# Kernel optimization log

Measured on AMD Instinct MI355X. Metric: run time of the kernel, lower is better.

Reference implementation:

```python
import jax, jax.numpy as jnp
import numpy as np

HEAD_SIZE = 128
N_EMBD = 64
B, T = 8, 4096


def setup_inputs() -> dict:
    key = jax.random.key(0)
    k1, k2, k3, k4 = jax.random.split(key, 4)
    x = jax.random.normal(k1, (B, T, N_EMBD), dtype=jnp.float32)
    Wq = jax.random.normal(k2, (N_EMBD, HEAD_SIZE), dtype=jnp.float32) * (N_EMBD ** -0.5)
    Wk = jax.random.normal(k3, (N_EMBD, HEAD_SIZE), dtype=jnp.float32) * (N_EMBD ** -0.5)
    Wv = jax.random.normal(k4, (N_EMBD, HEAD_SIZE), dtype=jnp.float32) * (N_EMBD ** -0.5)
    return {"x": x, "Wq": Wq, "Wk": Wk, "Wv": Wv}


def reference(x, Wq, Wk, Wv):
    # x: [B, T, C]; single-head causal self-attention (nanoGPT Head)
    q = x @ Wq  # [B, T, H]
    k = x @ Wk  # [B, T, H]
    v = x @ Wv  # [B, T, H]
    scale = HEAD_SIZE ** -0.5
    scores = jnp.einsum("bth,bsh->bts", q, k) * scale  # [B, T, T]
    t = x.shape[1]
    causal = jnp.tril(jnp.ones((t, t), dtype=bool))  # [T, T]
    scores = jnp.where(causal[None, :, :], scores, jnp.float32(-jnp.inf))
    wei = jax.nn.softmax(scores, axis=-1)  # [B, T, T]; dropout p=0.0 -> identity
    out = jnp.einsum("bts,bsh->bth", wei, v)  # [B, T, H]
    return out
```

## Files before the change

kernel.cpp:

```cpp
#include <hip/hip_runtime.h>
#include <math.h>

#define BB 8
#define TT 4096
#define CC 64
#define HH 128
#define NTH 256
#define XSTR 72
#define WSTR 72
#define QSCALE ((float)(0.08838834764831845 * 1.4426950408889634))

typedef __attribute__((ext_vector_type(8)))  short short8;
typedef __attribute__((ext_vector_type(4)))  float floatx4;
typedef __attribute__((ext_vector_type(16))) float floatx16;

__device__ __forceinline__ unsigned short f2bf(float f) {
    union { float f; unsigned int u; } un; un.f = f;
    unsigned int r = un.u + 0x7FFF + ((un.u >> 16) & 1);
    return (unsigned short)(r >> 16);
}
__device__ __forceinline__ unsigned int pack2bf(float a, float b) {
    return (unsigned int)f2bf(a) | ((unsigned int)f2bf(b) << 16);
}
__device__ __forceinline__ float bflo(unsigned int u) {
    union { unsigned int u; float f; } x; x.u = u << 16; return x.f;
}
__device__ __forceinline__ float bfhi(unsigned int u) {
    union { unsigned int u; float f; } x; x.u = u & 0xffff0000u; return x.f;
}

__global__ __launch_bounds__(NTH) void qkv_mfma(
    const float* __restrict__ x,
    const float* __restrict__ Wq, const float* __restrict__ Wk, const float* __restrict__ Wv,
    unsigned short* __restrict__ qb, unsigned short* __restrict__ Kf,
    unsigned short* __restrict__ Vf)
{
    __shared__ __align__(16) unsigned short xs[64 * XSTR];
    __shared__ __align__(16) unsigned short Wts[3 * HH * WSTR];

    const int tid  = threadIdx.x;
    const int w    = tid >> 6;
    const int lane = tid & 63;
    const int quad = lane >> 4;
    const int lr   = lane & 15;

    const int b    = blockIdx.x >> 6;
    const int kblk = blockIdx.x & 63;
    const int t0   = kblk * 64;
    const long long rbase = (long long)b * TT + t0;

#pragma unroll
    for (int i = 0; i < 4; ++i) {
        const int idx = tid + i * NTH;
        const int r = idx >> 4, c4 = idx & 15;
        const float4 v = *(const float4*)(x + (rbase + r) * CC + c4 * 4);
        unsigned short tmp[4] = { f2bf(v.x), f2bf(v.y), f2bf(v.z), f2bf(v.w) };
        *(unsigned long long*)&xs[r * XSTR + c4 * 4] = *(unsigned long long*)tmp;
    }
#pragma unroll
    for (int mat = 0; mat < 3; ++mat) {
        const float* W = mat == 0 ? Wq : (mat == 1 ? Wk : Wv);
        const float s = mat == 0 ? QSCALE : 1.0f;
#pragma unroll
        for (int i = 0; i < 32; ++i) {
            const int idx = tid + i * NTH;
            const int c = idx >> 7, h = idx & 127;
            Wts[(mat * HH + h) * WSTR + c] = f2bf(W[idx] * s);
        }
    }
    __syncthreads();

    const short8 bx0 = *(const short8*)&xs[(w * 16 + lr) * XSTR + quad * 8];
    const short8 bx1 = *(const short8*)&xs[(w * 16 + lr) * XSTR + 32 + quad * 8];

    {
        const unsigned short* Wrow = Wts;
#pragma unroll
        for (int ht = 0; ht < 8; ++ht) {
            const short8 aw0 = *(const short8*)(Wrow + (ht * 16 + lr) * WSTR + quad * 8);
            const short8 aw1 = *(const short8*)(Wrow + (ht * 16 + lr) * WSTR + 32 + quad * 8);
            floatx4 acc = (floatx4)0.f;
            acc = __builtin_amdgcn_mfma_f32_16x16x32_bf16(aw0, bx0, acc, 0, 0, 0);
            acc = __builtin_amdgcn_mfma_f32_16x16x32_bf16(aw1, bx1, acc, 0, 0, 0);
            ushort4 st = { f2bf(acc[0]), f2bf(acc[1]), f2bf(acc[2]), f2bf(acc[3]) };
            *(ushort4*)(qb + (rbase + w * 16 + lr) * HH + ht * 16 + quad * 4) = st;
        }
    }
    {
        const unsigned short* Wrow = Wts + 1 * HH * WSTR;
        const int khp = w >> 1;
        const int lqp = (w & 1) * 16 + lr;
        unsigned short* kdst = Kf + ((long long)((b * 64 + kblk) * 2 + khp)) * 4096
                             + ((quad >> 1) & 1) * 256 + lqp * 8 + (quad & 1) * 4;
#pragma unroll
        for (int ht = 0; ht < 8; ++ht) {
            const short8 aw0 = *(const short8*)(Wrow + (ht * 16 + lr) * WSTR + quad * 8);
            const short8 aw1 = *(const short8*)(Wrow + (ht * 16 + lr) * WSTR + 32 + quad * 8);
            floatx4 acc = (floatx4)0.f;
            acc = __builtin_amdgcn_mfma_f32_16x16x32_bf16(aw0, bx0, acc, 0, 0, 0);
            acc = __builtin_amdgcn_mfma_f32_16x16x32_bf16(aw1, bx1, acc, 0, 0, 0);
            ushort4 st = { f2bf(acc[0]), f2bf(acc[1]), f2bf(acc[2]), f2bf(acc[3]) };
            *(ushort4*)(kdst + ht * 512) = st;
        }
    }
    {
        const unsigned short* Wrow = Wts + 2 * HH * WSTR;
        const int khv = w >> 1, ksv = w & 1, lsv = (quad >> 1) & 1;
        unsigned short* vdst = Vf + (long long)(b * 64 + kblk) * 8192 + khv * 4096
                             + ksv * 512 + lsv * 256 + (quad & 1) * 4;
#pragma unroll
        for (int htp = 0; htp < 8; ++htp) {
            const short8 bw0 = *(const short8*)(Wrow + (htp * 16 + lr) * WSTR + quad * 8);
            const short8 bw1 = *(const short8*)(Wrow + (htp * 16 + lr) * WSTR + 32 + quad * 8);
            floatx4 acc = (floatx4)0.f;
            acc = __builtin_amdgcn_mfma_f32_16x16x32_bf16(bx0, bw0, acc, 0, 0, 0);
            acc = __builtin_amdgcn_mfma_f32_16x16x32_bf16(bx1, bw1, acc, 0, 0, 0);
            ushort4 st = { f2bf(acc[0]), f2bf(acc[1]), f2bf(acc[2]), f2bf(acc[3]) };
            *(ushort4*)(vdst + (htp >> 1) * 1024 + ((htp & 1) * 16 + lr) * 8) = st;
        }
    }
}

__global__ __launch_bounds__(NTH, 2) void flash_splitk(
    const unsigned short* __restrict__ qb,
    const unsigned short* __restrict__ Kf,
    const unsigned short* __restrict__ Vf,
    unsigned short* __restrict__ Ob, float* __restrict__ Lb)
{
    __shared__ __align__(16) float ex[2][64 * 68];
    __shared__ float Lx[4][32];

    const int tid  = threadIdx.x;
    const int w    = tid >> 6;
    const int lane = tid & 63;
    const int lq   = lane & 31;
    const int ls   = lane >> 5;
    const int kh   = w & 1;
    const int qh   = w >> 1;

    const int id  = blockIdx.x;
    const int qt  = 63 - (id >> 5);
    const int b   = (id >> 2) & 7;
    const int c   = id & 3;
    const int len = (qt + 4) >> 2;
    const int lo  = c * len;
    if (lo > qt) return;
    const int hi  = (lo + len - 1 < qt) ? (lo + len - 1) : qt;

    const int q0 = qt * 64;
    const long long baset = (long long)b * TT;

    const unsigned short* kptr = Kf + ((long long)(b * 128 + kh)) * 4096 + lane * 8;
    const unsigned short* vptr = Vf + ((long long)b * 64) * 8192 + kh * 4096 + lane * 8;

    short8 aq[8];
    {
        const unsigned short* qrp = qb + (baset + q0 + qh * 32 + lq) * HH + ls * 8;
#pragma unroll
        for (int st = 0; st < 8; ++st)
            aq[st] = *(const short8*)(qrp + st * 16);
    }

    floatx16 o_acc[4];
#pragma unroll
    for (int ht = 0; ht < 4; ++ht) o_acc[ht] = (floatx16)0.f;
    float l_lane = 0.f;

    for (int kt = lo; kt <= hi; ++kt) {
        const unsigned short* kp = kptr + (long long)kt * 8192;
        const unsigned short* vp = vptr + (long long)kt * 8192;

        short8 kfr[8], vfr[8];
#pragma unroll
        for (int st = 0; st < 8; ++st)
            kfr[st] = *(const short8*)(kp + st * 512);
#pragma unroll
        for (int i = 0; i < 8; ++i)
            vfr[i] = *(const short8*)(vp + (i >> 1) * 1024 + (i & 1) * 512);

        const bool diag = (kt == qt);
        if (diag && kh > qh) continue;

        floatx16 s_acc = (floatx16)0.f;
#pragma unroll
        for (int st = 0; st < 8; ++st)
            s_acc = __builtin_amdgcn_mfma_f32_32x32x16_bf16(kfr[st], aq[st], s_acc, 0, 0, 0);

        float p[16];
        if (diag && kh == qh) {
#pragma unroll
            for (int reg = 0; reg < 16; ++reg) {
                const int kk = (reg & 3) + 8 * (reg >> 2) + 4 * ls;
                p[reg] = (kk <= lq) ? exp2f(s_acc[reg]) : 0.f;
            }
        } else {
#pragma unroll
            for (int reg = 0; reg < 16; ++reg)
                p[reg] = exp2f(s_acc[reg]);
        }
#pragma unroll
        for (int reg = 0; reg < 16; ++reg) l_lane += p[reg];

        unsigned int g[8], pg[8];
#pragma unroll
        for (int i = 0; i < 8; ++i) g[i] = pack2bf(p[2 * i], p[2 * i + 1]);
#pragma unroll
        for (int i = 0; i < 8; ++i) pg[i] = __shfl_xor((int)g[i], 32);
        short8 bp[2];
#pragma unroll
        for (int ks = 0; ks < 2; ++ks) {
            union { short8 s; unsigned int u[4]; } fr;
            const int bs = ks * 4;
            if (ls == 0) {
                fr.u[0] = g[bs];      fr.u[1] = g[bs + 1];
                fr.u[2] = pg[bs];     fr.u[3] = pg[bs + 1];
            } else {
                fr.u[0] = pg[bs + 2]; fr.u[1] = pg[bs + 3];
                fr.u[2] = g[bs + 2];  fr.u[3] = g[bs + 3];
            }
            bp[ks] = fr.s;
        }

#pragma unroll
        for (int ht = 0; ht < 4; ++ht) {
            o_acc[ht] = __builtin_amdgcn_mfma_f32_32x32x16_bf16(vfr[ht * 2 + 0], bp[0], o_acc[ht], 0, 0, 0);
            o_acc[ht] = __builtin_amdgcn_mfma_f32_32x32x16_bf16(vfr[ht * 2 + 1], bp[1], o_acc[ht], 0, 0, 0);
        }
    }

    const float l2 = l_lane + __shfl_xor(l_lane, 32);
    if (lane < 32) Lx[w][lq] = l2;
    if (kh == 1) {
        float* e = &ex[qh][lane * 68];
#pragma unroll
        for (int ht = 0; ht < 4; ++ht)
#pragma unroll
            for (int rg = 0; rg < 4; ++rg) {
                float4 v = make_float4(o_acc[ht][rg * 4 + 0], o_acc[ht][rg * 4 + 1],
                                       o_acc[ht][rg * 4 + 2], o_acc[ht][rg * 4 + 3]);
                *(float4*)&e[ht * 16 + rg * 4] = v;
            }
    }
    __syncthreads();
    if (kh == 0) {
        const int pid = ((b * 64 + qt) << 2) + c;
        Lb[pid * 64 + qh * 32 + lq] = Lx[2 * qh][lq] + Lx[2 * qh + 1][lq];
        const float* e = &ex[qh][lane * 68];
        unsigned short* od = Ob + (long long)pid * 8192 + (qh * 32 + lq) * HH;
#pragma unroll
        for (int ht = 0; ht < 4; ++ht)
#pragma unroll
            for (int rg = 0; rg < 4; ++rg) {
                const float4 pv = *(const float4*)&e[ht * 16 + rg * 4];
                ushort4 st = { f2bf(o_acc[ht][rg * 4 + 0] + pv.x),
                               f2bf(o_acc[ht][rg * 4 + 1] + pv.y),
                               f2bf(o_acc[ht][rg * 4 + 2] + pv.z),
                               f2bf(o_acc[ht][rg * 4 + 3] + pv.w) };
                *(ushort4*)(od + ht * 32 + rg * 8 + 4 * ls) = st;
            }
    }
}

__global__ __launch_bounds__(NTH) void combine(
    const unsigned short* __restrict__ Ob, const float* __restrict__ Lb,
    float* __restrict__ out)
{
    const int id = blockIdx.x;
    const int b = id & 7, qt = id >> 3;
    const int len = (qt + 4) >> 2;
    const int tid = threadIdx.x;
    const int q = tid >> 2;
    const int hg = tid & 3;
    const int pid0 = (b * 64 + qt) << 2;

    float acc[32];
#pragma unroll
    for (int i = 0; i < 32; ++i) acc[i] = 0.f;
    float ltot = 0.f;

#pragma unroll
    for (int c = 0; c < 4; ++c) {
        if (c * len > qt) break;
        ltot += Lb[(pid0 + c) * 64 + q];
        const uint4* src = (const uint4*)(Ob + (long long)(pid0 + c) * 8192 + q * HH + hg * 32);
#pragma unroll
        for (int g = 0; g < 4; ++g) {
            const uint4 d = src[g];
            acc[g * 8 + 0] += bflo(d.x); acc[g * 8 + 1] += bfhi(d.x);
            acc[g * 8 + 2] += bflo(d.y); acc[g * 8 + 3] += bfhi(d.y);
            acc[g * 8 + 4] += bflo(d.z); acc[g * 8 + 5] += bfhi(d.z);
            acc[g * 8 + 6] += bflo(d.w); acc[g * 8 + 7] += bfhi(d.w);
        }
    }
    const float inv = 1.f / ltot;
    float* op = out + ((long long)b * TT + qt * 64 + q) * HH + hg * 32;
#pragma unroll
    for (int g = 0; g < 8; ++g) {
        float4 st = make_float4(acc[g * 4 + 0] * inv, acc[g * 4 + 1] * inv,
                                acc[g * 4 + 2] * inv, acc[g * 4 + 3] * inv);
        *(float4*)(op + g * 4) = st;
    }
}

extern "C" void kernel_launch(void* const* d_in, const int* in_sizes, int n_in,
                              void* d_out, int out_size, void* d_ws, size_t ws_size,
                              hipStream_t stream)
{
    const float* x  = (const float*)d_in[0];
    const float* Wq = (const float*)d_in[1];
    const float* Wk = (const float*)d_in[2];
    const float* Wv = (const float*)d_in[3];
    float* out = (float*)d_out;

    const long long n = (long long)BB * TT * HH;
    unsigned short* qb = (unsigned short*)d_ws;
    unsigned short* Kf = qb + n;
    unsigned short* Vf = Kf + n;
    unsigned short* Ob = Vf + n;
    float*          Lb = (float*)(Ob + (long long)2048 * 8192);

    qkv_mfma<<<BB * (TT / 64), NTH, 0, stream>>>(x, Wq, Wk, Wv, qb, Kf, Vf);
    flash_splitk<<<2048, NTH, 0, stream>>>(qb, Kf, Vf, Ob, Lb);
    combine<<<BB * 64, NTH, 0, stream>>>(Ob, Lb, out);
}
```

Baseline: 162.8 us.

## Double-buffer K/V tiles in LDS via async global-to-LDS loads with 128-row query tiles

The split-K flash kernel now uses 512-thread blocks covering 128 query rows, so each K/V tile is staged once into LDS and shared by twice as many query rows. Tiles are loaded with async global_load_lds into a double buffer, prefetching the next tile while the current one is computed. The causal mask is generalized to per-warp diagonal offsets, and the bf16 packing uses a cheaper perm-based round. The cost is more LDS per block, a barrier every iteration, and slightly different rounding on P and partial outputs.

```diff
diff --git a/kernel.cpp b/kernel.cpp
--- a/kernel.cpp
+++ b/kernel.cpp
@@ -19,14 +19,21 @@
     unsigned int r = un.u + 0x7FFF + ((un.u >> 16) & 1);
     return (unsigned short)(r >> 16);
 }
-__device__ __forceinline__ unsigned int pack2bf(float a, float b) {
-    return (unsigned int)f2bf(a) | ((unsigned int)f2bf(b) << 16);
+__device__ __forceinline__ unsigned int pack2bf_fast(float a, float b) {
+    union { float f; unsigned int u; } ua, ub; ua.f = a; ub.f = b;
+    return __builtin_amdgcn_perm(ub.u + 0x8000u, ua.u + 0x8000u, 0x07060302u);
 }
 __device__ __forceinline__ float bflo(unsigned int u) {
     union { unsigned int u; float f; } x; x.u = u << 16; return x.f;
 }
 __device__ __forceinline__ float bfhi(unsigned int u) {
     union { unsigned int u; float f; } x; x.u = u & 0xffff0000u; return x.f;
+}
+
+__device__ __forceinline__ void gl_lds16(const void* g, void* l) {
+    __builtin_amdgcn_global_load_lds(
+        (const __attribute__((address_space(1))) unsigned int*)g,
+        (__attribute__((address_space(3))) unsigned int*)l, 16, 0, 0);
 }
 
 __global__ __launch_bounds__(NTH) void qkv_mfma(
@@ -121,14 +128,32 @@
     }
 }
 
-__global__ __launch_bounds__(NTH, 2) void flash_splitk(
+__device__ __forceinline__ void dma_tile(
+    const unsigned char* __restrict__ Ksrc, const unsigned char* __restrict__ Vsrc,
+    long long kt, unsigned char* buf, int w, int lane)
+{
+    const unsigned char* src;
+    unsigned char* dst;
+    if (w < 4) {
+        src = Ksrc + kt * 16384 + w * 4096 + lane * 16;
+        dst = buf + w * 4096;
+    } else {
+        src = Vsrc + kt * 16384 + (w - 4) * 4096 + lane * 16;
+        dst = buf + 16384 + (w - 4) * 4096;
+    }
+#pragma unroll
+    for (int i = 0; i < 4; ++i)
+        gl_lds16(src + i * 1024, dst + i * 1024);
+}
+
+__global__ __launch_bounds__(512, 4) void flash_splitk(
     const unsigned short* __restrict__ qb,
     const unsigned short* __restrict__ Kf,
     const unsigned short* __restrict__ Vf,
     unsigned short* __restrict__ Ob, float* __restrict__ Lb)
 {
-    __shared__ __align__(16) float ex[2][64 * 68];
-    __shared__ float Lx[4][32];
+    __shared__ __align__(16) unsigned char KV[2][32768];
+    __shared__ float Lx[8][32];
 
     const int tid  = threadIdx.x;
     const int w    = tid >> 6;
@@ -138,20 +163,24 @@
     const int kh   = w & 1;
     const int qh   = w >> 1;
 
-    const int id  = blockIdx.x;
-    const int qt  = 63 - (id >> 5);
-    const int b   = (id >> 2) & 7;
-    const int c   = id & 3;
-    const int len = (qt + 4) >> 2;
-    const int lo  = c * len;
-    if (lo > qt) return;
-    const int hi  = (lo + len - 1 < qt) ? (lo + len - 1) : qt;
-
-    const int q0 = qt * 64;
+    const int id     = blockIdx.x;
+    const int qtile  = 31 - (id >> 5);
+    const int rem    = id & 31;
+    const int b      = rem >> 2;
+    const int c      = rem & 3;
+    const int ntiles = 2 * qtile + 2;
+    const int len    = (ntiles + 3) >> 2;
+    const int lo     = c * len;
+    if (lo >= ntiles) return;
+    const int hi0 = lo + len - 1;
+    const int hi  = hi0 < ntiles - 1 ? hi0 : ntiles - 1;
+
+    const int q0 = qtile * 128;
     const long long baset = (long long)b * TT;
-
-    const unsigned short* kptr = Kf + ((long long)(b * 128 + kh)) * 4096 + lane * 8;
-    const unsigned short* vptr = Vf + ((long long)b * 64) * 8192 + kh * 4096 + lane * 8;
+    const unsigned char* Ksrc = (const unsigned char*)Kf + (long long)(b * 64) * 16384;
+    const unsigned char* Vsrc = (const unsigned char*)Vf + (long long)(b * 64) * 16384;
+
+    dma_tile(Ksrc, Vsrc, lo, KV[0], w, lane);
 
     short8 aq[8];
     {
@@ -167,71 +196,78 @@
     float l_lane = 0.f;
 
     for (int kt = lo; kt <= hi; ++kt) {
-        const unsigned short* kp = kptr + (long long)kt * 8192;
-        const unsigned short* vp = vptr + (long long)kt * 8192;
-
-        short8 kfr[8], vfr[8];
-#pragma unroll
-        for (int st = 0; st < 8; ++st)
-            kfr[st] = *(const short8*)(kp + st * 512);
-#pragma unroll
-        for (int i = 0; i < 8; ++i)
-            vfr[i] = *(const short8*)(vp + (i >> 1) * 1024 + (i & 1) * 512);
-
-        const bool diag = (kt == qt);
-        if (diag && kh > qh) continue;
-
-        floatx16 s_acc = (floatx16)0.f;
-#pragma unroll
-        for (int st = 0; st < 8; ++st)
-            s_acc = __builtin_amdgcn_mfma_f32_32x32x16_bf16(kfr[st], aq[st], s_acc, 0, 0, 0);
-
-        float p[16];
-        if (diag && kh == qh) {
-#pragma unroll
-            for (int reg = 0; reg < 16; ++reg) {
-                const int kk = (reg & 3) + 8 * (reg >> 2) + 4 * ls;
-                p[reg] = (kk <= lq) ? exp2f(s_acc[reg]) : 0.f;
-            }
-        } else {
-#pragma unroll
-            for (int reg = 0; reg < 16; ++reg)
-                p[reg] = exp2f(s_acc[reg]);
-        }
-#pragma unroll
-        for (int reg = 0; reg < 16; ++reg) l_lane += p[reg];
-
-        unsigned int g[8], pg[8];
-#pragma unroll
-        for (int i = 0; i < 8; ++i) g[i] = pack2bf(p[2 * i], p[2 * i + 1]);
-#pragma unroll
-        for (int i = 0; i < 8; ++i) pg[i] = __shfl_xor((int)g[i], 32);
-        short8 bp[2];
-#pragma unroll
-        for (int ks = 0; ks < 2; ++ks) {
-            union { short8 s; unsigned int u[4]; } fr;
-            const int bs = ks * 4;
-            if (ls == 0) {
-                fr.u[0] = g[bs];      fr.u[1] = g[bs + 1];
-                fr.u[2] = pg[bs];     fr.u[3] = pg[bs + 1];
+        const int cb = (kt - lo) & 1;
+        __syncthreads();
+        if (kt < hi)
+            dma_tile(Ksrc, Vsrc, kt + 1, KV[cb ^ 1], w, lane);
+
+        const int D = q0 + qh * 32 - kt * 64 - kh * 32;
+        if (D > -32) {
+            const unsigned short* Kt = (const unsigned short*)&KV[cb][0]     + kh * 4096;
+            const unsigned short* Vt = (const unsigned short*)&KV[cb][16384] + kh * 4096;
+
+            short8 kfr[8], vfr[8];
+#pragma unroll
+            for (int st = 0; st < 8; ++st)
+                kfr[st] = *(const short8*)(Kt + st * 512 + lane * 8);
+#pragma unroll
+            for (int i = 0; i < 8; ++i)
+                vfr[i] = *(const short8*)(Vt + (i >> 1) * 1024 + (i & 1) * 512 + lane * 8);
+
+            floatx16 s_acc = (floatx16)0.f;
+#pragma unroll
+            for (int st = 0; st < 8; ++st)
+                s_acc = __builtin_amdgcn_mfma_f32_32x32x16_bf16(kfr[st], aq[st], s_acc, 0, 0, 0);
+
+            float p[16];
+            if (D < 31) {
+#pragma unroll
+                for (int reg = 0; reg < 16; ++reg) {
+                    const int kk = (reg & 3) + 8 * (reg >> 2) + 4 * ls;
+                    p[reg] = (kk <= lq + D) ? exp2f(s_acc[reg]) : 0.f;
+                }
             } else {
-                fr.u[0] = pg[bs + 2]; fr.u[1] = pg[bs + 3];
-                fr.u[2] = g[bs + 2];  fr.u[3] = g[bs + 3];
-            }
-            bp[ks] = fr.s;
-        }
-
-#pragma unroll
-        for (int ht = 0; ht < 4; ++ht) {
-            o_acc[ht] = __builtin_amdgcn_mfma_f32_32x32x16_bf16(vfr[ht * 2 + 0], bp[0], o_acc[ht], 0, 0, 0);
-            o_acc[ht] = __builtin_amdgcn_mfma_f32_32x32x16_bf16(vfr[ht * 2 + 1], bp[1], o_acc[ht], 0, 0, 0);
+#pragma unroll
+                for (int reg = 0; reg < 16; ++reg)
+                    p[reg] = exp2f(s_acc[reg]);
+            }
+#pragma unroll
+            for (int reg = 0; reg < 16; ++reg) l_lane += p[reg];
+
+            unsigned int g[8], pg[8];
+#pragma unroll
+            for (int i = 0; i < 8; ++i) g[i] = pack2bf_fast(p[2 * i], p[2 * i + 1]);
+#pragma unroll
+            for (int i = 0; i < 8; ++i) pg[i] = __shfl_xor((int)g[i], 32);
+            short8 bp[2];
+#pragma unroll
+            for (int ks = 0; ks < 2; ++ks) {
+                union { short8 s; unsigned int u[4]; } fr;
+                const int bs = ks * 4;
+                if (ls == 0) {
+                    fr.u[0] = g[bs];      fr.u[1] = g[bs + 1];
+                    fr.u[2] = pg[bs];     fr.u[3] = pg[bs + 1];
+                } else {
+                    fr.u[0] = pg[bs + 2]; fr.u[1] = pg[bs + 3];
+                    fr.u[2] = g[bs + 2];  fr.u[3] = g[bs + 3];
+                }
+                bp[ks] = fr.s;
+            }
+
+#pragma unroll
+            for (int ht = 0; ht < 4; ++ht) {
+                o_acc[ht] = __builtin_amdgcn_mfma_f32_32x32x16_bf16(vfr[ht * 2 + 0], bp[0], o_acc[ht], 0, 0, 0);
+                o_acc[ht] = __builtin_amdgcn_mfma_f32_32x32x16_bf16(vfr[ht * 2 + 1], bp[1], o_acc[ht], 0, 0, 0);
+            }
         }
     }
 
     const float l2 = l_lane + __shfl_xor(l_lane, 32);
     if (lane < 32) Lx[w][lq] = l2;
+    __syncthreads();
+    float* ex = (float*)&KV[0][0] + qh * 4096;
     if (kh == 1) {
-        float* e = &ex[qh][lane * 68];
+        float* e = ex + lane * 64;
 #pragma unroll
         for (int ht = 0; ht < 4; ++ht)
 #pragma unroll
@@ -243,20 +279,19 @@
     }
     __syncthreads();
     if (kh == 0) {
-        const int pid = ((b * 64 + qt) << 2) + c;
-        Lb[pid * 64 + qh * 32 + lq] = Lx[2 * qh][lq] + Lx[2 * qh + 1][lq];
-        const float* e = &ex[qh][lane * 68];
-        unsigned short* od = Ob + (long long)pid * 8192 + (qh * 32 + lq) * HH;
+        const int pid = ((b * 32 + qtile) << 2) + c;
+        Lb[pid * 128 + qh * 32 + lq] = Lx[2 * qh][lq] + Lx[2 * qh + 1][lq];
+        const float* e = ex + lane * 64;
+        unsigned short* od = Ob + (long long)pid * 16384 + (qh * 32 + lq) * HH;
 #pragma unroll
         for (int ht = 0; ht < 4; ++ht)
 #pragma unroll
             for (int rg = 0; rg < 4; ++rg) {
                 const float4 pv = *(const float4*)&e[ht * 16 + rg * 4];
-                ushort4 st = { f2bf(o_acc[ht][rg * 4 + 0] + pv.x),
-                               f2bf(o_acc[ht][rg * 4 + 1] + pv.y),
-                               f2bf(o_acc[ht][rg * 4 + 2] + pv.z),
-                               f2bf(o_acc[ht][rg * 4 + 3] + pv.w) };
-                *(ushort4*)(od + ht * 32 + rg * 8 + 4 * ls) = st;
+                uint2 st;
+                st.x = pack2bf_fast(o_acc[ht][rg * 4 + 0] + pv.x, o_acc[ht][rg * 4 + 1] + pv.y);
+                st.y = pack2bf_fast(o_acc[ht][rg * 4 + 2] + pv.z, o_acc[ht][rg * 4 + 3] + pv.w);
+                *(uint2*)(od + ht * 32 + rg * 8 + 4 * ls) = st;
             }
     }
 }
@@ -266,12 +301,14 @@
     float* __restrict__ out)
 {
     const int id = blockIdx.x;
-    const int b = id & 7, qt = id >> 3;
-    const int len = (qt + 4) >> 2;
+    const int b = id & 7, qt64 = id >> 3;
+    const int qtile = qt64 >> 1, sub = qt64 & 1;
+    const int ntiles = 2 * qtile + 2;
+    const int len = (ntiles + 3) >> 2;
     const int tid = threadIdx.x;
     const int q = tid >> 2;
     const int hg = tid & 3;
-    const int pid0 = (b * 64 + qt) << 2;
+    const int pid0 = (b * 32 + qtile) << 2;
 
     float acc[32];
 #pragma unroll
@@ -280,9 +317,10 @@
 
 #pragma unroll
     for (int c = 0; c < 4; ++c) {
-        if (c * len > qt) break;
-        ltot += Lb[(pid0 + c) * 64 + q];
-        const uint4* src = (const uint4*)(Ob + (long long)(pid0 + c) * 8192 + q * HH + hg * 32);
+        if (c * len >= ntiles) break;
+        ltot += Lb[(pid0 + c) * 128 + sub * 64 + q];
+        const uint4* src = (const uint4*)(Ob + (long long)(pid0 + c) * 16384
+                                          + (sub * 64 + q) * HH + hg * 32);
 #pragma unroll
         for (int g = 0; g < 4; ++g) {
             const uint4 d = src[g];
@@ -293,7 +331,7 @@
         }
     }
     const float inv = 1.f / ltot;
-    float* op = out + ((long long)b * TT + qt * 64 + q) * HH + hg * 32;
+    float* op = out + ((long long)b * TT + qtile * 128 + sub * 64 + q) * HH + hg * 32;
 #pragma unroll
     for (int g = 0; g < 8; ++g) {
         float4 st = make_float4(acc[g * 4 + 0] * inv, acc[g * 4 + 1] * inv,
@@ -317,9 +355,9 @@
     unsigned short* Kf = qb + n;
     unsigned short* Vf = Kf + n;
     unsigned short* Ob = Vf + n;
-    float*          Lb = (float*)(Ob + (long long)2048 * 8192);
+    float*          Lb = (float*)(Ob + (long long)1024 * 16384);
 
     qkv_mfma<<<BB * (TT / 64), NTH, 0, stream>>>(x, Wq, Wk, Wv, qb, Kf, Vf);
-    flash_splitk<<<2048, NTH, 0, stream>>>(qb, Kf, Vf, Ob, Lb);
+    flash_splitk<<<1024, 512, 0, stream>>>(qb, Kf, Vf, Ob, Lb);
     combine<<<BB * 64, NTH, 0, stream>>>(Ob, Lb, out);
 }
```

Result: slower. 259.6 us (+59.5%).
